# Optimization experiments

Hardware: AMD Instinct MI355X
Metric: run time of the kernel (lower is better)

The kernel has to match this reference:

```python
import jax, jax.numpy as jnp
import numpy as np

N_NODES = 100000
N_EDGES = 1600000
IN_CH = 128
HID_CH = 128
EMB_CH = 128
OUT_CH = 64


def _sage_conv(x, src, dst, W_l, b_l, W_r):
    # PyG SAGEConv (mean aggr): out = lin_l(mean_{j->i} x_j) + lin_r(x_i)
    n = x.shape[0]
    msg = x[src]                                             # [E, d] gather
    summed = jax.ops.segment_sum(msg, dst, num_segments=n)   # [N, d]
    cnt = jax.ops.segment_sum(jnp.ones((src.shape[0],), x.dtype), dst, num_segments=n)
    mean = summed / jnp.maximum(cnt, 1.0)[:, None]
    return mean @ W_l + b_l + x @ W_r


def setup_inputs() -> dict:
    key = jax.random.key(0)
    ks = jax.random.split(key, 10)
    x = jax.random.normal(ks[0], (N_NODES, IN_CH), dtype=jnp.float32)
    edge_index = jax.random.randint(ks[1], (2, N_EDGES), 0, N_NODES, dtype=jnp.int32)
    s1 = 1.0 / np.sqrt(IN_CH)
    s2 = 1.0 / np.sqrt(HID_CH)
    s3 = 1.0 / np.sqrt(EMB_CH)
    return {
        "x": x,
        "edge_index": edge_index,
        "W1l": jax.random.uniform(ks[2], (IN_CH, HID_CH), jnp.float32, -s1, s1),
        "b1": jnp.zeros((HID_CH,), jnp.float32),
        "W1r": jax.random.uniform(ks[3], (IN_CH, HID_CH), jnp.float32, -s1, s1),
        "W2l": jax.random.uniform(ks[4], (HID_CH, EMB_CH), jnp.float32, -s2, s2),
        "b2": jnp.zeros((EMB_CH,), jnp.float32),
        "W2r": jax.random.uniform(ks[5], (HID_CH, EMB_CH), jnp.float32, -s2, s2),
        "Wm": jax.random.uniform(ks[6], (EMB_CH, OUT_CH), jnp.float32, -s3, s3),
        "bm": jax.random.uniform(ks[7], (OUT_CH,), jnp.float32, -s3, s3),
    }


def reference(x, edge_index, W1l, b1, W1r, W2l, b2, W2r, Wm, bm):
    src, dst = edge_index[0], edge_index[1]
    h = jax.nn.relu(_sage_conv(x, src, dst, W1l, b1, W1r))
    emb = _sage_conv(h, src, dst, W2l, b2, W2r)
    out = emb @ Wm + bm
    # F.normalize(emb, p=2, dim=-1)
    norm = jnp.sqrt(jnp.sum(emb * emb, axis=-1, keepdims=True))
    emb_n = emb / jnp.maximum(norm, 1e-12)
    return out, emb_n
```

## Files before the change

kernel.cpp:

```cpp
#include <hip/hip_runtime.h>
#include <hip/hip_fp16.h>
#include <cstdint>
#include <cstddef>

#define N_NODES 100000
#define N_EDGES 1600000
#define BSH 6
#define BNODES 64
#define NB 1563
#define CHUNK 2048

typedef _Float16 f16x8 __attribute__((ext_vector_type(8)));
typedef float f32x4 __attribute__((ext_vector_type(4)));


__device__ __forceinline__ float h2f(ushort u) {
    __half_raw r;
    r.x = u;
    return __half2float(__half(r));
}

__device__ __forceinline__ ushort f2h(float f) {
    __half h = __float2half(f);
    return static_cast<__half_raw>(h).x;
}

__device__ __forceinline__ void acc4(float4& a, uint2 v) {
    a.x += h2f((ushort)(v.x & 0xffff));
    a.y += h2f((ushort)(v.x >> 16));
    a.z += h2f((ushort)(v.y & 0xffff));
    a.w += h2f((ushort)(v.y >> 16));
}


__global__ __launch_bounds__(256) void prep_all(
        const int* __restrict__ dst, int* __restrict__ bcnt, int E,
        const float* __restrict__ x, ushort* __restrict__ x_f16, int n4,
        const float* __restrict__ W1l, const float* __restrict__ W1r,
        const float* __restrict__ W2l, const float* __restrict__ W2r,
        const float* __restrict__ Wm,
        ushort* __restrict__ W1lT, ushort* __restrict__ W1rT,
        ushort* __restrict__ W2lT, ushort* __restrict__ W2rT,
        ushort* __restrict__ WmT) {
    int bid = blockIdx.x;
    if (bid < 256) {
        __shared__ int lh[NB];
        for (int i = threadIdx.x; i < NB; i += 256) lh[i] = 0;
        __syncthreads();
        for (int e = bid * 256 + threadIdx.x; e < E; e += 256 * 256)
            atomicAdd(&lh[dst[e] >> BSH], 1);
        __syncthreads();
        for (int i = threadIdx.x; i < NB; i += 256) {
            int v = lh[i];
            if (v) atomicAdd(&bcnt[i], v);
        }
    } else if (bid < 256 + 12500) {
        int i = (bid - 256) * 256 + threadIdx.x;
        if (i < n4) {
            float4 v = reinterpret_cast<const float4*>(x)[i];
            ushort4 o;
            o.x = f2h(v.x);
            o.y = f2h(v.y);
            o.z = f2h(v.z);
            o.w = f2h(v.w);
            reinterpret_cast<ushort4*>(x_f16)[i] = o;
        }
    } else {
        int t = (bid - (256 + 12500)) * 256 + threadIdx.x;
        if (t < 65536) {
            int wsel = t >> 14;
            int r = t & 16383;
            const float* srcs[4] = {W1l, W1r, W2l, W2r};
            ushort* dsts[4] = {W1lT, W1rT, W2lT, W2rT};
            int k = r >> 7, c = r & 127;
            dsts[wsel][c * 128 + k] = f2h(srcs[wsel][r]);
        } else if (t < 65536 + 8192) {
            int r = t - 65536;
            int k = r >> 6, c = r & 63;
            WmT[c * 128 + k] = f2h(Wm[r]);
        }
    }
}

__global__ void scan_buckets(const int* __restrict__ bcnt, int* __restrict__ boffs) {
    __shared__ int sdata[256];
    int tid = threadIdx.x;
    int v[8];
    int s = 0;
#pragma unroll
    for (int i = 0; i < 8; i++) {
        int idx = tid * 8 + i;
        v[i] = (idx < NB) ? bcnt[idx] : 0;
        s += v[i];
    }
    sdata[tid] = s;
    __syncthreads();
    int acc = s;
    for (int off = 1; off < 256; off <<= 1) {
        int t = (tid >= off) ? sdata[tid - off] : 0;
        __syncthreads();
        acc += t;
        sdata[tid] = acc;
        __syncthreads();
    }
    int excl = acc - s;
#pragma unroll
    for (int i = 0; i < 8; i++) {
        int idx = tid * 8 + i;
        if (idx < NB) boffs[idx] = excl;
        excl += v[i];
    }
}

__global__ void bucket_scatter(const int* __restrict__ src, const int* __restrict__ dst,
                               const int* __restrict__ boffs, int* __restrict__ gcur,
                               uint* __restrict__ bedges, int E) {
    __shared__ int lh[NB];
    __shared__ int lbase[NB];
    int nwg = gridDim.x;
    int chunk = (E + nwg - 1) / nwg;
    int e0 = blockIdx.x * chunk;
    int e1 = e0 + chunk;
    if (e1 > E) e1 = E;
    for (int i = threadIdx.x; i < NB; i += 256) lh[i] = 0;
    __syncthreads();
    for (int e = e0 + threadIdx.x; e < e1; e += 256)
        atomicAdd(&lh[dst[e] >> BSH], 1);
    __syncthreads();
    for (int i = threadIdx.x; i < NB; i += 256) {
        int v = lh[i];
        lbase[i] = v ? (boffs[i] + atomicAdd(&gcur[i], v)) : 0;
    }
    __syncthreads();
    for (int i = threadIdx.x; i < NB; i += 256) lh[i] = 0;
    __syncthreads();
    int e = e0 + threadIdx.x;
#pragma unroll 1
    for (; e + 3 * 256 < e1; e += 4 * 256) {
        int d0 = dst[e + 0 * 256], s0 = src[e + 0 * 256];
        int d1 = dst[e + 1 * 256], s1 = src[e + 1 * 256];
        int d2 = dst[e + 2 * 256], s2 = src[e + 2 * 256];
        int d3 = dst[e + 3 * 256], s3 = src[e + 3 * 256];
        int b0 = d0 >> BSH, b1 = d1 >> BSH, b2 = d2 >> BSH, b3 = d3 >> BSH;
        int r0 = atomicAdd(&lh[b0], 1);
        int r1 = atomicAdd(&lh[b1], 1);
        int r2 = atomicAdd(&lh[b2], 1);
        int r3 = atomicAdd(&lh[b3], 1);
        bedges[lbase[b0] + r0] = ((uint)(d0 & (BNODES - 1)) << 17) | (uint)s0;
        bedges[lbase[b1] + r1] = ((uint)(d1 & (BNODES - 1)) << 17) | (uint)s1;
        bedges[lbase[b2] + r2] = ((uint)(d2 & (BNODES - 1)) << 17) | (uint)s2;
        bedges[lbase[b3] + r3] = ((uint)(d3 & (BNODES - 1)) << 17) | (uint)s3;
    }
    for (; e < e1; e += 256) {
        int d = dst[e];
        int b = d >> BSH;
        int r = atomicAdd(&lh[b], 1);
        bedges[lbase[b] + r] = ((uint)(d & (BNODES - 1)) << 17) | (uint)src[e];
    }
}


__global__ __launch_bounds__(512) void aggregate_bucket(
        const ushort* __restrict__ F, const uint* __restrict__ bedges,
        const int* __restrict__ boffs, const int* __restrict__ bcnt,
        ushort* __restrict__ out, int n) {
    int b = blockIdx.x;
    int beg = boffs[b];
    int m = bcnt[b];
    int node0 = b << BSH;
    int nNodes = n - node0;
    if (nNodes > BNODES) nNodes = BNODES;
    __shared__ uint ls[CHUNK];
    __shared__ int lh[BNODES];
    __shared__ int lofs[BNODES];
    __shared__ int pcnt[BNODES];
    int tid = threadIdx.x;
    int wid = tid >> 6;
    int lane = tid & 63;
    int hw = lane >> 5;
    int cl = lane & 31;

    float4 acc[8];
#pragma unroll
    for (int i = 0; i < 8; i++) acc[i] = make_float4(0.f, 0.f, 0.f, 0.f);
    if (tid < BNODES) pcnt[tid] = 0;

    for (int base = 0; base < m; base += CHUNK) {
        int mm = m - base;
        if (mm > CHUNK) mm = CHUNK;
        __syncthreads();
        if (tid < BNODES) lh[tid] = 0;
        __syncthreads();
        for (int i = tid; i < mm; i += 512)
            atomicAdd(&lh[bedges[beg + base + i] >> 17], 1);
        __syncthreads();
        if (tid < BNODES) {
            int v = lh[tid];
            int s = v;
#pragma unroll
            for (int off = 1; off < 64; off <<= 1) {
                int t = __shfl_up(s, off);
                if (lane >= off) s += t;
            }
            lofs[tid] = s - v;
            pcnt[tid] += v;
            lh[tid] = 0;
        }
        __syncthreads();
        for (int i = tid; i < mm; i += 512) {
            uint p = bedges[beg + base + i];
            int k = p >> 17;
            int r = atomicAdd(&lh[k], 1);
            ls[lofs[k] + r] = p;
        }
        __syncthreads();
#pragma unroll
        for (int ki = 0; ki < 8; ki++) {
            int k = wid * 8 + ki;
            int s0 = lofs[k];
            int ck = lh[k];
            int j = hw;
            for (; j + 6 < ck; j += 8) {
                uint p0 = ls[s0 + j + 0] & 0x1FFFFu;
                uint p1 = ls[s0 + j + 2] & 0x1FFFFu;
                uint p2 = ls[s0 + j + 4] & 0x1FFFFu;
                uint p3 = ls[s0 + j + 6] & 0x1FFFFu;
                uint2 v0 = *reinterpret_cast<const uint2*>(F + (size_t)p0 * 128 + cl * 4);
                uint2 v1 = *reinterpret_cast<const uint2*>(F + (size_t)p1 * 128 + cl * 4);
                uint2 v2 = *reinterpret_cast<const uint2*>(F + (size_t)p2 * 128 + cl * 4);
                uint2 v3 = *reinterpret_cast<const uint2*>(F + (size_t)p3 * 128 + cl * 4);
                acc4(acc[ki], v0);
                acc4(acc[ki], v1);
                acc4(acc[ki], v2);
                acc4(acc[ki], v3);
            }
            for (; j < ck; j += 2) {
                uint p = ls[s0 + j] & 0x1FFFFu;
                uint2 v = *reinterpret_cast<const uint2*>(F + (size_t)p * 128 + cl * 4);
                acc4(acc[ki], v);
            }
        }
    }
    __syncthreads();
#pragma unroll
    for (int ki = 0; ki < 8; ki++) {
        acc[ki].x += __shfl_xor(acc[ki].x, 32);
        acc[ki].y += __shfl_xor(acc[ki].y, 32);
        acc[ki].z += __shfl_xor(acc[ki].z, 32);
        acc[ki].w += __shfl_xor(acc[ki].w, 32);
    }
    if (hw == 0) {
#pragma unroll
        for (int ki = 0; ki < 8; ki++) {
            int k = wid * 8 + ki;
            if (k < nNodes) {
                float inv = 1.0f / fmaxf((float)pcnt[k], 1.0f);
                uint2 o;
                o.x = (uint)f2h(acc[ki].x * inv) | ((uint)f2h(acc[ki].y * inv) << 16);
                o.y = (uint)f2h(acc[ki].z * inv) | ((uint)f2h(acc[ki].w * inv) << 16);
                *reinterpret_cast<uint2*>(out + (size_t)(node0 + k) * 128 + cl * 4) = o;
            }
        }
    }
}


template <bool RELU>
__global__ __launch_bounds__(256) void mfma_gemm(const ushort* __restrict__ A1,
                                                 const ushort* __restrict__ B1T,
                                                 const ushort* __restrict__ A2,
                                                 const ushort* __restrict__ B2T,
                                                 const float* __restrict__ bias,
                                                 ushort* __restrict__ Ch, int n) {
    int wid = threadIdx.x >> 6;
    int lane = threadIdx.x & 63;
    int row0 = blockIdx.x * 128 + wid * 32;
    int fr = lane & 15;
    int ko = (lane >> 4) * 8;

    f32x4 acc[2][8];
#pragma unroll
    for (int m = 0; m < 2; m++)
#pragma unroll
        for (int nf = 0; nf < 8; nf++) acc[m][nf] = (f32x4)0.f;

    for (int seg = 0; seg < 2; ++seg) {
        const ushort* A = seg ? A2 : A1;
        const ushort* BT = seg ? B2T : B1T;
#pragma unroll
        for (int k0 = 0; k0 < 128; k0 += 32) {
            f16x8 av[2];
#pragma unroll
            for (int m = 0; m < 2; m++) {
                int row = row0 + m * 16 + fr;
                if (row >= n) row = n - 1;
                av[m] = *reinterpret_cast<const f16x8*>(A + (size_t)row * 128 + k0 + ko);
            }
            f16x8 bv[8];
#pragma unroll
            for (int nf = 0; nf < 8; nf++)
                bv[nf] = *reinterpret_cast<const f16x8*>(BT + (size_t)(nf * 16 + fr) * 128 + k0 + ko);
#pragma unroll
            for (int m = 0; m < 2; m++)
#pragma unroll
                for (int nf = 0; nf < 8; nf++)
                    acc[m][nf] = __builtin_amdgcn_mfma_f32_16x16x32_f16(av[m], bv[nf], acc[m][nf], 0, 0, 0);
        }
    }

    int crow = (lane >> 4) * 4;
    int ccol = lane & 15;
    float bv[8];
#pragma unroll
    for (int nf = 0; nf < 8; nf++) bv[nf] = bias[nf * 16 + ccol];

#pragma unroll
    for (int m = 0; m < 2; m++) {
#pragma unroll
        for (int reg = 0; reg < 4; reg++) {
            int grow = row0 + m * 16 + crow + reg;
            if (grow < n) {
#pragma unroll
                for (int nf = 0; nf < 8; nf++) {
                    float v = acc[m][nf][reg] + bv[nf];
                    if (RELU) v = fmaxf(v, 0.f);
                    Ch[(size_t)grow * 128 + nf * 16 + ccol] = f2h(v);
                }
            }
        }
    }
}


__global__ __launch_bounds__(256) void gemm2_fused(const ushort* __restrict__ A1,
                                                   const ushort* __restrict__ B1T,
                                                   const ushort* __restrict__ A2,
                                                   const ushort* __restrict__ B2T,
                                                   const float* __restrict__ bias,
                                                   const ushort* __restrict__ WmT,
                                                   const float* __restrict__ bm,
                                                   float* __restrict__ outp,
                                                   float* __restrict__ embn, int n) {
    constexpr int LDK = 136;
    __shared__ ushort et[128 * LDK];
    int wid = threadIdx.x >> 6;
    int lane = threadIdx.x & 63;
    int row0 = blockIdx.x * 128 + wid * 32;
    int fr = lane & 15;
    int ko = (lane >> 4) * 8;

    f32x4 acc[2][8];
#pragma unroll
    for (int m = 0; m < 2; m++)
#pragma unroll
        for (int nf = 0; nf < 8; nf++) acc[m][nf] = (f32x4)0.f;

    for (int seg = 0; seg < 2; ++seg) {
        const ushort* A = seg ? A2 : A1;
        const ushort* BT = seg ? B2T : B1T;
#pragma unroll
        for (int k0 = 0; k0 < 128; k0 += 32) {
            f16x8 av[2];
#pragma unroll
            for (int m = 0; m < 2; m++) {
                int row = row0 + m * 16 + fr;
                if (row >= n) row = n - 1;
                av[m] = *reinterpret_cast<const f16x8*>(A + (size_t)row * 128 + k0 + ko);
            }
            f16x8 bv[8];
#pragma unroll
            for (int nf = 0; nf < 8; nf++)
                bv[nf] = *reinterpret_cast<const f16x8*>(BT + (size_t)(nf * 16 + fr) * 128 + k0 + ko);
#pragma unroll
            for (int m = 0; m < 2; m++)
#pragma unroll
                for (int nf = 0; nf < 8; nf++)
                    acc[m][nf] = __builtin_amdgcn_mfma_f32_16x16x32_f16(av[m], bv[nf], acc[m][nf], 0, 0, 0);
        }
    }

    int crow = (lane >> 4) * 4;
    int ccol = lane & 15;
    float bvv[8];
#pragma unroll
    for (int nf = 0; nf < 8; nf++) bvv[nf] = bias[nf * 16 + ccol];

#pragma unroll
    for (int m = 0; m < 2; m++) {
#pragma unroll
        for (int reg = 0; reg < 4; reg++) {
            float vv[8];
            float ss = 0.f;
#pragma unroll
            for (int nf = 0; nf < 8; nf++) {
                float v = acc[m][nf][reg] + bvv[nf];
                vv[nf] = v;
                ss += v * v;
            }
            ss += __shfl_xor(ss, 1);
            ss += __shfl_xor(ss, 2);
            ss += __shfl_xor(ss, 4);
            ss += __shfl_xor(ss, 8);
            float inv = 1.0f / fmaxf(sqrtf(ss), 1e-12f);
            int lrow = wid * 32 + m * 16 + crow + reg;
            int grow = blockIdx.x * 128 + lrow;
#pragma unroll
            for (int nf = 0; nf < 8; nf++)
                et[lrow * LDK + nf * 16 + ccol] = f2h(vv[nf]);
            if (grow < n) {
#pragma unroll
                for (int nf = 0; nf < 8; nf++)
                    embn[(size_t)grow * 128 + nf * 16 + ccol] = vv[nf] * inv;
            }
        }
    }
    __syncthreads();

    f32x4 acc2[2][4];
#pragma unroll
    for (int m = 0; m < 2; m++)
#pragma unroll
        for (int nf = 0; nf < 4; nf++) acc2[m][nf] = (f32x4)0.f;

#pragma unroll
    for (int k0 = 0; k0 < 128; k0 += 32) {
        f16x8 av[2];
#pragma unroll
        for (int m = 0; m < 2; m++) {
            int lrow = wid * 32 + m * 16 + fr;
            av[m] = *reinterpret_cast<const f16x8*>(&et[lrow * LDK + k0 + ko]);
        }
        f16x8 bv[4];
#pragma unroll
        for (int nf = 0; nf < 4; nf++)
            bv[nf] = *reinterpret_cast<const f16x8*>(WmT + (size_t)(nf * 16 + fr) * 128 + k0 + ko);
#pragma unroll
        for (int m = 0; m < 2; m++)
#pragma unroll
            for (int nf = 0; nf < 4; nf++)
                acc2[m][nf] = __builtin_amdgcn_mfma_f32_16x16x32_f16(av[m], bv[nf], acc2[m][nf], 0, 0, 0);
    }

#pragma unroll
    for (int m = 0; m < 2; m++) {
#pragma unroll
        for (int reg = 0; reg < 4; reg++) {
            int grow = row0 + m * 16 + crow + reg;
            if (grow < n) {
#pragma unroll
                for (int nf = 0; nf < 4; nf++)
                    outp[(size_t)grow * 64 + nf * 16 + ccol] = acc2[m][nf][reg] + bm[nf * 16 + ccol];
            }
        }
    }
}


extern "C" void kernel_launch(void* const* d_in, const int* in_sizes, int n_in,
                              void* d_out, int out_size, void* d_ws, size_t ws_size,
                              hipStream_t stream) {
    const float* x   = (const float*)d_in[0];
    const int*   ei  = (const int*)d_in[1];
    const float* W1l = (const float*)d_in[2];
    const float* b1  = (const float*)d_in[3];
    const float* W1r = (const float*)d_in[4];
    const float* W2l = (const float*)d_in[5];
    const float* b2  = (const float*)d_in[6];
    const float* W2r = (const float*)d_in[7];
    const float* Wm  = (const float*)d_in[8];
    const float* bm  = (const float*)d_in[9];

    const int N = N_NODES, E = N_EDGES;
    const int* src = ei;
    const int* dst = ei + E;

    char* ws = (char*)d_ws;
    int* bcnt  = (int*)ws;  ws += sizeof(int) * NB;
    int* boffs = (int*)ws;  ws += sizeof(int) * NB;
    int* gcur  = (int*)ws;  ws += sizeof(int) * NB;
    uintptr_t p0 = ((uintptr_t)ws + 255) & ~(uintptr_t)255;
    uint* bedges = (uint*)p0;
    uintptr_t p1 = ((uintptr_t)(bedges + N_EDGES) + 255) & ~(uintptr_t)255;
    ushort* mean_f16 = (ushort*)p1;
    ushort* x_f16    = mean_f16 + (size_t)N * 128;
    ushort* h_f16    = x_f16 + (size_t)N * 128;
    ushort* W1lT     = h_f16 + (size_t)N * 128;
    ushort* W1rT     = W1lT + 128 * 128;
    ushort* W2lT     = W1rT + 128 * 128;
    ushort* W2rT     = W2lT + 128 * 128;
    ushort* WmT      = W2rT + 128 * 128;

    float* outp = (float*)d_out;
    float* embn = outp + (size_t)N * 64;

    hipMemsetAsync(bcnt, 0, sizeof(int) * NB, stream);
    hipMemsetAsync(gcur, 0, sizeof(int) * NB, stream);

    int n4 = N * 128 / 4;
    int prep_blocks = 256 + 12500 + 288;
    prep_all<<<prep_blocks, 256, 0, stream>>>(dst, bcnt, E, x, x_f16, n4,
                                              W1l, W1r, W2l, W2r, Wm,
                                              W1lT, W1rT, W2lT, W2rT, WmT);
    scan_buckets<<<1, 256, 0, stream>>>(bcnt, boffs);
    bucket_scatter<<<256, 256, 0, stream>>>(src, dst, boffs, gcur, bedges, E);

    int gblk = (N + 127) / 128;

    aggregate_bucket<<<NB, 512, 0, stream>>>(x_f16, bedges, boffs, bcnt, mean_f16, N);
    mfma_gemm<true><<<gblk, 256, 0, stream>>>(mean_f16, W1lT, x_f16, W1rT, b1, h_f16, N);

    aggregate_bucket<<<NB, 512, 0, stream>>>(h_f16, bedges, boffs, bcnt, mean_f16, N);
    gemm2_fused<<<gblk, 256, 0, stream>>>(mean_f16, W2lT, h_f16, W2rT, b2,
                                          WmT, bm, outp, embn, N);
}
```

Measured before the change: 323.7 us.

## Fuse neighbor mean aggregation with SAGE GEMMs via LDS tiles

Each bucket block now aggregates its 64 nodes' neighbor means into an LDS tile and immediately runs the lin_l/lin_r MFMA GEMMs, bias and ReLU (layer 1), or bias, L2 normalize and the output projection (layer 2). This removes the mean_f16 round trip through global memory and two kernel launches. In exchange, the aggregation blocks grow in LDS and register use, which may lower occupancy for the gather-bound phase. Weights are also re-read per 64-node block instead of per 128-row block.

```diff
diff --git a/kernel.cpp b/kernel.cpp
--- a/kernel.cpp
+++ b/kernel.cpp
@@ -9,6 +9,7 @@
 #define BNODES 64
 #define NB 1563
 #define CHUNK 2048
+#define LDK 136
 
 typedef _Float16 f16x8 __attribute__((ext_vector_type(8)));
 typedef float f32x4 __attribute__((ext_vector_type(4)));
@@ -160,20 +161,9 @@
 }
 
 
-__global__ __launch_bounds__(512) void aggregate_bucket(
+__device__ __forceinline__ void aggregate_to_lds(
         const ushort* __restrict__ F, const uint* __restrict__ bedges,
-        const int* __restrict__ boffs, const int* __restrict__ bcnt,
-        ushort* __restrict__ out, int n) {
-    int b = blockIdx.x;
-    int beg = boffs[b];
-    int m = bcnt[b];
-    int node0 = b << BSH;
-    int nNodes = n - node0;
-    if (nNodes > BNODES) nNodes = BNODES;
-    __shared__ uint ls[CHUNK];
-    __shared__ int lh[BNODES];
-    __shared__ int lofs[BNODES];
-    __shared__ int pcnt[BNODES];
+        int beg, int m, ushort* mt, uint* ls, int* lh, int* lofs, int* pcnt) {
     int tid = threadIdx.x;
     int wid = tid >> 6;
     int lane = tid & 63;
@@ -253,203 +243,207 @@
 #pragma unroll
         for (int ki = 0; ki < 8; ki++) {
             int k = wid * 8 + ki;
-            if (k < nNodes) {
-                float inv = 1.0f / fmaxf((float)pcnt[k], 1.0f);
-                uint2 o;
-                o.x = (uint)f2h(acc[ki].x * inv) | ((uint)f2h(acc[ki].y * inv) << 16);
-                o.y = (uint)f2h(acc[ki].z * inv) | ((uint)f2h(acc[ki].w * inv) << 16);
-                *reinterpret_cast<uint2*>(out + (size_t)(node0 + k) * 128 + cl * 4) = o;
-            }
-        }
-    }
-}
-
-
-template <bool RELU>
-__global__ __launch_bounds__(256) void mfma_gemm(const ushort* __restrict__ A1,
-                                                 const ushort* __restrict__ B1T,
-                                                 const ushort* __restrict__ A2,
-                                                 const ushort* __restrict__ B2T,
-                                                 const float* __restrict__ bias,
-                                                 ushort* __restrict__ Ch, int n) {
+            float inv = 1.0f / fmaxf((float)pcnt[k], 1.0f);
+            uint2 o;
+            o.x = (uint)f2h(acc[ki].x * inv) | ((uint)f2h(acc[ki].y * inv) << 16);
+            o.y = (uint)f2h(acc[ki].z * inv) | ((uint)f2h(acc[ki].w * inv) << 16);
+            *reinterpret_cast<uint2*>(&mt[k * LDK + cl * 4]) = o;
+        }
+    }
+    __syncthreads();
+}
+
+
+__global__ __launch_bounds__(512) void agg_gemm1(
+        const ushort* __restrict__ x_f16, const uint* __restrict__ bedges,
+        const int* __restrict__ boffs, const int* __restrict__ bcnt,
+        const ushort* __restrict__ W1lT, const ushort* __restrict__ W1rT,
+        const float* __restrict__ b1, ushort* __restrict__ h_f16, int n) {
+    __shared__ uint ls[CHUNK];
+    __shared__ int lh[BNODES];
+    __shared__ int lofs[BNODES];
+    __shared__ int pcnt[BNODES];
+    __shared__ ushort mt[BNODES * LDK];
+    int b = blockIdx.x;
+    int node0 = b << BSH;
+    aggregate_to_lds(x_f16, bedges, boffs[b], bcnt[b], mt, ls, lh, lofs, pcnt);
+
     int wid = threadIdx.x >> 6;
     int lane = threadIdx.x & 63;
-    int row0 = blockIdx.x * 128 + wid * 32;
+    int rt = wid & 3;
+    int cg = wid >> 2;
     int fr = lane & 15;
     int ko = (lane >> 4) * 8;
 
-    f32x4 acc[2][8];
-#pragma unroll
-    for (int m = 0; m < 2; m++)
-#pragma unroll
-        for (int nf = 0; nf < 8; nf++) acc[m][nf] = (f32x4)0.f;
-
-    for (int seg = 0; seg < 2; ++seg) {
-        const ushort* A = seg ? A2 : A1;
-        const ushort* BT = seg ? B2T : B1T;
+    f32x4 acc[4];
+#pragma unroll
+    for (int nf = 0; nf < 4; nf++) acc[nf] = (f32x4)0.f;
+
+#pragma unroll
+    for (int k0 = 0; k0 < 128; k0 += 32) {
+        f16x8 av = *reinterpret_cast<const f16x8*>(&mt[(rt * 16 + fr) * LDK + k0 + ko]);
+#pragma unroll
+        for (int nf = 0; nf < 4; nf++) {
+            f16x8 bv = *reinterpret_cast<const f16x8*>(
+                W1lT + (size_t)(cg * 64 + nf * 16 + fr) * 128 + k0 + ko);
+            acc[nf] = __builtin_amdgcn_mfma_f32_16x16x32_f16(av, bv, acc[nf], 0, 0, 0);
+        }
+    }
+    {
+        int grow = node0 + rt * 16 + fr;
+        if (grow >= n) grow = n - 1;
 #pragma unroll
         for (int k0 = 0; k0 < 128; k0 += 32) {
-            f16x8 av[2];
-#pragma unroll
-            for (int m = 0; m < 2; m++) {
-                int row = row0 + m * 16 + fr;
-                if (row >= n) row = n - 1;
-                av[m] = *reinterpret_cast<const f16x8*>(A + (size_t)row * 128 + k0 + ko);
-            }
-            f16x8 bv[8];
-#pragma unroll
-            for (int nf = 0; nf < 8; nf++)
-                bv[nf] = *reinterpret_cast<const f16x8*>(BT + (size_t)(nf * 16 + fr) * 128 + k0 + ko);
-#pragma unroll
-            for (int m = 0; m < 2; m++)
-#pragma unroll
-                for (int nf = 0; nf < 8; nf++)
-                    acc[m][nf] = __builtin_amdgcn_mfma_f32_16x16x32_f16(av[m], bv[nf], acc[m][nf], 0, 0, 0);
+            f16x8 av = *reinterpret_cast<const f16x8*>(x_f16 + (size_t)grow * 128 + k0 + ko);
+#pragma unroll
+            for (int nf = 0; nf < 4; nf++) {
+                f16x8 bv = *reinterpret_cast<const f16x8*>(
+                    W1rT + (size_t)(cg * 64 + nf * 16 + fr) * 128 + k0 + ko);
+                acc[nf] = __builtin_amdgcn_mfma_f32_16x16x32_f16(av, bv, acc[nf], 0, 0, 0);
+            }
         }
     }
 
     int crow = (lane >> 4) * 4;
     int ccol = lane & 15;
-    float bv[8];
-#pragma unroll
-    for (int nf = 0; nf < 8; nf++) bv[nf] = bias[nf * 16 + ccol];
-
-#pragma unroll
-    for (int m = 0; m < 2; m++) {
-#pragma unroll
-        for (int reg = 0; reg < 4; reg++) {
-            int grow = row0 + m * 16 + crow + reg;
-            if (grow < n) {
-#pragma unroll
-                for (int nf = 0; nf < 8; nf++) {
-                    float v = acc[m][nf][reg] + bv[nf];
-                    if (RELU) v = fmaxf(v, 0.f);
-                    Ch[(size_t)grow * 128 + nf * 16 + ccol] = f2h(v);
-                }
-            }
-        }
-    }
-}
-
-
-__global__ __launch_bounds__(256) void gemm2_fused(const ushort* __restrict__ A1,
-                                                   const ushort* __restrict__ B1T,
-                                                   const ushort* __restrict__ A2,
-                                                   const ushort* __restrict__ B2T,
-                                                   const float* __restrict__ bias,
-                                                   const ushort* __restrict__ WmT,
-                                                   const float* __restrict__ bm,
-                                                   float* __restrict__ outp,
-                                                   float* __restrict__ embn, int n) {
-    constexpr int LDK = 136;
-    __shared__ ushort et[128 * LDK];
-    int wid = threadIdx.x >> 6;
-    int lane = threadIdx.x & 63;
-    int row0 = blockIdx.x * 128 + wid * 32;
+#pragma unroll
+    for (int reg = 0; reg < 4; reg++) {
+        int grow = node0 + rt * 16 + crow + reg;
+        if (grow < n) {
+#pragma unroll
+            for (int nf = 0; nf < 4; nf++) {
+                float v = acc[nf][reg] + b1[cg * 64 + nf * 16 + ccol];
+                v = fmaxf(v, 0.f);
+                h_f16[(size_t)grow * 128 + cg * 64 + nf * 16 + ccol] = f2h(v);
+            }
+        }
+    }
+}
+
+
+__global__ __launch_bounds__(512) void agg_gemm2(
+        const ushort* __restrict__ h_f16, const uint* __restrict__ bedges,
+        const int* __restrict__ boffs, const int* __restrict__ bcnt,
+        const ushort* __restrict__ W2lT, const ushort* __restrict__ W2rT,
+        const float* __restrict__ b2, const ushort* __restrict__ WmT,
+        const float* __restrict__ bm, float* __restrict__ outp,
+        float* __restrict__ embn, int n) {
+    __shared__ uint ls[CHUNK];
+    __shared__ int lh[BNODES];
+    __shared__ int lofs[BNODES];
+    __shared__ int pcnt[BNODES];
+    __shared__ ushort mt[BNODES * LDK];
+    __shared__ ushort et[BNODES * LDK];
+    int b = blockIdx.x;
+    int node0 = b << BSH;
+    aggregate_to_lds(h_f16, bedges, boffs[b], bcnt[b], mt, ls, lh, lofs, pcnt);
+
+    int tid = threadIdx.x;
+    int wid = tid >> 6;
+    int lane = tid & 63;
+    int rt = wid & 3;
+    int cg = wid >> 2;
     int fr = lane & 15;
     int ko = (lane >> 4) * 8;
 
-    f32x4 acc[2][8];
-#pragma unroll
-    for (int m = 0; m < 2; m++)
-#pragma unroll
-        for (int nf = 0; nf < 8; nf++) acc[m][nf] = (f32x4)0.f;
-
-    for (int seg = 0; seg < 2; ++seg) {
-        const ushort* A = seg ? A2 : A1;
-        const ushort* BT = seg ? B2T : B1T;
+    f32x4 acc[4];
+#pragma unroll
+    for (int nf = 0; nf < 4; nf++) acc[nf] = (f32x4)0.f;
+
+#pragma unroll
+    for (int k0 = 0; k0 < 128; k0 += 32) {
+        f16x8 av = *reinterpret_cast<const f16x8*>(&mt[(rt * 16 + fr) * LDK + k0 + ko]);
+#pragma unroll
+        for (int nf = 0; nf < 4; nf++) {
+            f16x8 bv = *reinterpret_cast<const f16x8*>(
+                W2lT + (size_t)(cg * 64 + nf * 16 + fr) * 128 + k0 + ko);
+            acc[nf] = __builtin_amdgcn_mfma_f32_16x16x32_f16(av, bv, acc[nf], 0, 0, 0);
+        }
+    }
+    {
+        int grow = node0 + rt * 16 + fr;
+        if (grow >= n) grow = n - 1;
 #pragma unroll
         for (int k0 = 0; k0 < 128; k0 += 32) {
-            f16x8 av[2];
-#pragma unroll
-            for (int m = 0; m < 2; m++) {
-                int row = row0 + m * 16 + fr;
-                if (row >= n) row = n - 1;
-                av[m] = *reinterpret_cast<const f16x8*>(A + (size_t)row * 128 + k0 + ko);
-            }
-            f16x8 bv[8];
-#pragma unroll
-            for (int nf = 0; nf < 8; nf++)
-                bv[nf] = *reinterpret_cast<const f16x8*>(BT + (size_t)(nf * 16 + fr) * 128 + k0 + ko);
-#pragma unroll
-            for (int m = 0; m < 2; m++)
-#pragma unroll
-                for (int nf = 0; nf < 8; nf++)
-                    acc[m][nf] = __builtin_amdgcn_mfma_f32_16x16x32_f16(av[m], bv[nf], acc[m][nf], 0, 0, 0);
+            f16x8 av = *reinterpret_cast<const f16x8*>(h_f16 + (size_t)grow * 128 + k0 + ko);
+#pragma unroll
+            for (int nf = 0; nf < 4; nf++) {
+                f16x8 bv = *reinterpret_cast<const f16x8*>(
+                    W2rT + (size_t)(cg * 64 + nf * 16 + fr) * 128 + k0 + ko);
+                acc[nf] = __builtin_amdgcn_mfma_f32_16x16x32_f16(av, bv, acc[nf], 0, 0, 0);
+            }
         }
     }
 
     int crow = (lane >> 4) * 4;
     int ccol = lane & 15;
-    float bvv[8];
-#pragma unroll
-    for (int nf = 0; nf < 8; nf++) bvv[nf] = bias[nf * 16 + ccol];
-
-#pragma unroll
-    for (int m = 0; m < 2; m++) {
+#pragma unroll
+    for (int reg = 0; reg < 4; reg++) {
+        int lrow = rt * 16 + crow + reg;
+#pragma unroll
+        for (int nf = 0; nf < 4; nf++) {
+            float v = acc[nf][reg] + b2[cg * 64 + nf * 16 + ccol];
+            et[lrow * LDK + cg * 64 + nf * 16 + ccol] = f2h(v);
+        }
+    }
+    __syncthreads();
+
+    {
+        int row = tid >> 3;
+        int p = tid & 7;
+        f16x8 e0 = *reinterpret_cast<const f16x8*>(&et[row * LDK + p * 16]);
+        f16x8 e1 = *reinterpret_cast<const f16x8*>(&et[row * LDK + p * 16 + 8]);
+        float vals[16];
+        float ss = 0.f;
+#pragma unroll
+        for (int j = 0; j < 8; j++) {
+            vals[j] = (float)e0[j];
+            vals[8 + j] = (float)e1[j];
+        }
+#pragma unroll
+        for (int j = 0; j < 16; j++) ss += vals[j] * vals[j];
+        ss += __shfl_xor(ss, 1);
+        ss += __shfl_xor(ss, 2);
+        ss += __shfl_xor(ss, 4);
+        float inv = 1.0f / fmaxf(sqrtf(ss), 1e-12f);
+        int grow = node0 + row;
+        if (grow < n) {
+            float4 o0, o1, o2, o3;
+            o0.x = vals[0] * inv;  o0.y = vals[1] * inv;  o0.z = vals[2] * inv;  o0.w = vals[3] * inv;
+            o1.x = vals[4] * inv;  o1.y = vals[5] * inv;  o1.z = vals[6] * inv;  o1.w = vals[7] * inv;
+            o2.x = vals[8] * inv;  o2.y = vals[9] * inv;  o2.z = vals[10] * inv; o2.w = vals[11] * inv;
+            o3.x = vals[12] * inv; o3.y = vals[13] * inv; o3.z = vals[14] * inv; o3.w = vals[15] * inv;
+            float* dst = embn + (size_t)grow * 128 + p * 16;
+            *reinterpret_cast<float4*>(dst + 0) = o0;
+            *reinterpret_cast<float4*>(dst + 4) = o1;
+            *reinterpret_cast<float4*>(dst + 8) = o2;
+            *reinterpret_cast<float4*>(dst + 12) = o3;
+        }
+    }
+
+    {
+        int ct2 = (wid >> 2) * 2;
+        f32x4 acc3[2];
+        acc3[0] = (f32x4)0.f;
+        acc3[1] = (f32x4)0.f;
+#pragma unroll
+        for (int k0 = 0; k0 < 128; k0 += 32) {
+            f16x8 av = *reinterpret_cast<const f16x8*>(&et[(rt * 16 + fr) * LDK + k0 + ko]);
+#pragma unroll
+            for (int nf = 0; nf < 2; nf++) {
+                f16x8 bv = *reinterpret_cast<const f16x8*>(
+                    WmT + (size_t)((ct2 + nf) * 16 + fr) * 128 + k0 + ko);
+                acc3[nf] = __builtin_amdgcn_mfma_f32_16x16x32_f16(av, bv, acc3[nf], 0, 0, 0);
+            }
+        }
 #pragma unroll
         for (int reg = 0; reg < 4; reg++) {
-            float vv[8];
-            float ss = 0.f;
-#pragma unroll
-            for (int nf = 0; nf < 8; nf++) {
-                float v = acc[m][nf][reg] + bvv[nf];
-                vv[nf] = v;
-                ss += v * v;
-            }
-            ss += __shfl_xor(ss, 1);
-            ss += __shfl_xor(ss, 2);
-            ss += __shfl_xor(ss, 4);
-            ss += __shfl_xor(ss, 8);
-            float inv = 1.0f / fmaxf(sqrtf(ss), 1e-12f);
-            int lrow = wid * 32 + m * 16 + crow + reg;
-            int grow = blockIdx.x * 128 + lrow;
-#pragma unroll
-            for (int nf = 0; nf < 8; nf++)
-                et[lrow * LDK + nf * 16 + ccol] = f2h(vv[nf]);
+            int grow = node0 + rt * 16 + crow + reg;
             if (grow < n) {
 #pragma unroll
-                for (int nf = 0; nf < 8; nf++)
-                    embn[(size_t)grow * 128 + nf * 16 + ccol] = vv[nf] * inv;
-            }
-        }
-    }
-    __syncthreads();
-
-    f32x4 acc2[2][4];
-#pragma unroll
-    for (int m = 0; m < 2; m++)
-#pragma unroll
-        for (int nf = 0; nf < 4; nf++) acc2[m][nf] = (f32x4)0.f;
-
-#pragma unroll
-    for (int k0 = 0; k0 < 128; k0 += 32) {
-        f16x8 av[2];
-#pragma unroll
-        for (int m = 0; m < 2; m++) {
-            int lrow = wid * 32 + m * 16 + fr;
-            av[m] = *reinterpret_cast<const f16x8*>(&et[lrow * LDK + k0 + ko]);
-        }
-        f16x8 bv[4];
-#pragma unroll
-        for (int nf = 0; nf < 4; nf++)
-            bv[nf] = *reinterpret_cast<const f16x8*>(WmT + (size_t)(nf * 16 + fr) * 128 + k0 + ko);
-#pragma unroll
-        for (int m = 0; m < 2; m++)
-#pragma unroll
-            for (int nf = 0; nf < 4; nf++)
-                acc2[m][nf] = __builtin_amdgcn_mfma_f32_16x16x32_f16(av[m], bv[nf], acc2[m][nf], 0, 0, 0);
-    }
-
-#pragma unroll
-    for (int m = 0; m < 2; m++) {
-#pragma unroll
-        for (int reg = 0; reg < 4; reg++) {
-            int grow = row0 + m * 16 + crow + reg;
-            if (grow < n) {
-#pragma unroll
-                for (int nf = 0; nf < 4; nf++)
-                    outp[(size_t)grow * 64 + nf * 16 + ccol] = acc2[m][nf][reg] + bm[nf * 16 + ccol];
+                for (int nf = 0; nf < 2; nf++)
+                    outp[(size_t)grow * 64 + (ct2 + nf) * 16 + ccol] =
+                        acc3[nf][reg] + bm[(ct2 + nf) * 16 + ccol];
             }
         }
     }
@@ -481,14 +475,13 @@
     uintptr_t p0 = ((uintptr_t)ws + 255) & ~(uintptr_t)255;
     uint* bedges = (uint*)p0;
     uintptr_t p1 = ((uintptr_t)(bedges + N_EDGES) + 255) & ~(uintptr_t)255;
-    ushort* mean_f16 = (ushort*)p1;
-    ushort* x_f16    = mean_f16 + (size_t)N * 128;
-    ushort* h_f16    = x_f16 + (size_t)N * 128;
-    ushort* W1lT     = h_f16 + (size_t)N * 128;
-    ushort* W1rT     = W1lT + 128 * 128;
-    ushort* W2lT     = W1rT + 128 * 128;
-    ushort* W2rT     = W2lT + 128 * 128;
-    ushort* WmT      = W2rT + 128 * 128;
+    ushort* x_f16 = (ushort*)p1;
+    ushort* h_f16 = x_f16 + (size_t)N * 128;
+    ushort* W1lT  = h_f16 + (size_t)N * 128;
+    ushort* W1rT  = W1lT + 128 * 128;
+    ushort* W2lT  = W1rT + 128 * 128;
+    ushort* W2rT  = W2lT + 128 * 128;
+    ushort* WmT   = W2rT + 128 * 128;
 
     float* outp = (float*)d_out;
     float* embn = outp + (size_t)N * 64;
@@ -504,12 +497,9 @@
     scan_buckets<<<1, 256, 0, stream>>>(bcnt, boffs);
     bucket_scatter<<<256, 256, 0, stream>>>(src, dst, boffs, gcur, bedges, E);
 
-    int gblk = (N + 127) / 128;
-
-    aggregate_bucket<<<NB, 512, 0, stream>>>(x_f16, bedges, boffs, bcnt, mean_f16, N);
-    mfma_gemm<true><<<gblk, 256, 0, stream>>>(mean_f16, W1lT, x_f16, W1rT, b1, h_f16, N);
-
-    aggregate_bucket<<<NB, 512, 0, stream>>>(h_f16, bedges, boffs, bcnt, mean_f16, N);
-    gemm2_fused<<<gblk, 256, 0, stream>>>(mean_f16, W2lT, h_f16, W2rT, b2,
-                                          WmT, bm, outp, embn, N);
-}
+    agg_gemm1<<<NB, 512, 0, stream>>>(x_f16, bedges, boffs, bcnt,
+                                      W1lT, W1rT, b1, h_f16, N);
+
+    agg_gemm2<<<NB, 512, 0, stream>>>(h_f16, bedges, boffs, bcnt,
+                                      W2lT, W2rT, b2, WmT, bm, outp, embn, N);
+}
```

Measured after the change: 358.5 us. 10.7% more time.

## Pre-pack weights in MFMA fragment order and halve GEMM row tiles

Applied to the files above, without the earlier changes.

Weights are now repacked during prep into the exact per-lane fragment order the 16x16x32 MFMA expects, so each B fragment load is a contiguous 16-byte load per lane rather than a strided row read. The GEMM kernels also change from 32 rows per wave (128 per block) to 16 rows per wave (64 per block), which doubles the grid and cuts accumulator registers. The aim is better occupancy and coalesced weight loads. The cost is that weight fragments are reloaded twice as often relative to the work done, since each wave now covers fewer rows.

```diff
diff --git a/kernel.cpp b/kernel.cpp
--- a/kernel.cpp
+++ b/kernel.cpp
@@ -9,6 +9,7 @@
 #define BNODES 64
 #define NB 1563
 #define CHUNK 2048
+#define LDK 136
 
 typedef _Float16 f16x8 __attribute__((ext_vector_type(8)));
 typedef float f32x4 __attribute__((ext_vector_type(4)));
@@ -39,9 +40,9 @@
         const float* __restrict__ W1l, const float* __restrict__ W1r,
         const float* __restrict__ W2l, const float* __restrict__ W2r,
         const float* __restrict__ Wm,
-        ushort* __restrict__ W1lT, ushort* __restrict__ W1rT,
-        ushort* __restrict__ W2lT, ushort* __restrict__ W2rT,
-        ushort* __restrict__ WmT) {
+        ushort* __restrict__ W1lP, ushort* __restrict__ W1rP,
+        ushort* __restrict__ W2lP, ushort* __restrict__ W2rP,
+        ushort* __restrict__ WmP) {
     int bid = blockIdx.x;
     if (bid < 256) {
         __shared__ int lh[NB];
@@ -69,15 +70,25 @@
         int t = (bid - (256 + 12500)) * 256 + threadIdx.x;
         if (t < 65536) {
             int wsel = t >> 14;
-            int r = t & 16383;
+            int o = t & 16383;
             const float* srcs[4] = {W1l, W1r, W2l, W2r};
-            ushort* dsts[4] = {W1lT, W1rT, W2lT, W2rT};
-            int k = r >> 7, c = r & 127;
-            dsts[wsel][c * 128 + k] = f2h(srcs[wsel][r]);
+            ushort* dsts[4] = {W1lP, W1rP, W2lP, W2rP};
+            int j = o & 7;
+            int lane = (o >> 3) & 63;
+            int kg = (o >> 9) & 3;
+            int nf = o >> 11;
+            int k = kg * 32 + (lane >> 4) * 8 + j;
+            int c = nf * 16 + (lane & 15);
+            dsts[wsel][o] = f2h(srcs[wsel][k * 128 + c]);
         } else if (t < 65536 + 8192) {
-            int r = t - 65536;
-            int k = r >> 6, c = r & 63;
-            WmT[c * 128 + k] = f2h(Wm[r]);
+            int o = t - 65536;
+            int j = o & 7;
+            int lane = (o >> 3) & 63;
+            int kg = (o >> 9) & 3;
+            int nf = o >> 11;
+            int k = kg * 32 + (lane >> 4) * 8 + j;
+            int c = nf * 16 + (lane & 15);
+            WmP[o] = f2h(Wm[k * 64 + c]);
         }
     }
 }
@@ -265,192 +276,135 @@
 }
 
 
-template <bool RELU>
-__global__ __launch_bounds__(256) void mfma_gemm(const ushort* __restrict__ A1,
-                                                 const ushort* __restrict__ B1T,
-                                                 const ushort* __restrict__ A2,
-                                                 const ushort* __restrict__ B2T,
-                                                 const float* __restrict__ bias,
-                                                 ushort* __restrict__ Ch, int n) {
+__global__ __launch_bounds__(256) void gemm1(
+        const ushort* __restrict__ A1, const ushort* __restrict__ W1lP,
+        const ushort* __restrict__ A2, const ushort* __restrict__ W1rP,
+        const float* __restrict__ b1, ushort* __restrict__ h_f16, int n) {
     int wid = threadIdx.x >> 6;
     int lane = threadIdx.x & 63;
-    int row0 = blockIdx.x * 128 + wid * 32;
+    int row0 = blockIdx.x * 64 + wid * 16;
     int fr = lane & 15;
     int ko = (lane >> 4) * 8;
-
-    f32x4 acc[2][8];
-#pragma unroll
-    for (int m = 0; m < 2; m++)
-#pragma unroll
-        for (int nf = 0; nf < 8; nf++) acc[m][nf] = (f32x4)0.f;
+    int arow = row0 + fr;
+    if (arow >= n) arow = n - 1;
+
+    f32x4 acc[8];
+#pragma unroll
+    for (int nf = 0; nf < 8; nf++) acc[nf] = (f32x4)0.f;
 
     for (int seg = 0; seg < 2; ++seg) {
         const ushort* A = seg ? A2 : A1;
-        const ushort* BT = seg ? B2T : B1T;
-#pragma unroll
-        for (int k0 = 0; k0 < 128; k0 += 32) {
-            f16x8 av[2];
-#pragma unroll
-            for (int m = 0; m < 2; m++) {
-                int row = row0 + m * 16 + fr;
-                if (row >= n) row = n - 1;
-                av[m] = *reinterpret_cast<const f16x8*>(A + (size_t)row * 128 + k0 + ko);
-            }
-            f16x8 bv[8];
-#pragma unroll
-            for (int nf = 0; nf < 8; nf++)
-                bv[nf] = *reinterpret_cast<const f16x8*>(BT + (size_t)(nf * 16 + fr) * 128 + k0 + ko);
-#pragma unroll
-            for (int m = 0; m < 2; m++)
-#pragma unroll
-                for (int nf = 0; nf < 8; nf++)
-                    acc[m][nf] = __builtin_amdgcn_mfma_f32_16x16x32_f16(av[m], bv[nf], acc[m][nf], 0, 0, 0);
+        const ushort* WP = seg ? W1rP : W1lP;
+#pragma unroll
+        for (int kg = 0; kg < 4; kg++) {
+            f16x8 av = *reinterpret_cast<const f16x8*>(A + (size_t)arow * 128 + kg * 32 + ko);
+#pragma unroll
+            for (int nf = 0; nf < 8; nf++) {
+                f16x8 bv = *reinterpret_cast<const f16x8*>(WP + (nf * 4 + kg) * 512 + lane * 8);
+                acc[nf] = __builtin_amdgcn_mfma_f32_16x16x32_f16(av, bv, acc[nf], 0, 0, 0);
+            }
         }
     }
 
     int crow = (lane >> 4) * 4;
     int ccol = lane & 15;
-    float bv[8];
-#pragma unroll
-    for (int nf = 0; nf < 8; nf++) bv[nf] = bias[nf * 16 + ccol];
-
-#pragma unroll
-    for (int m = 0; m < 2; m++) {
-#pragma unroll
-        for (int reg = 0; reg < 4; reg++) {
-            int grow = row0 + m * 16 + crow + reg;
-            if (grow < n) {
-#pragma unroll
-                for (int nf = 0; nf < 8; nf++) {
-                    float v = acc[m][nf][reg] + bv[nf];
-                    if (RELU) v = fmaxf(v, 0.f);
-                    Ch[(size_t)grow * 128 + nf * 16 + ccol] = f2h(v);
-                }
-            }
-        }
-    }
-}
-
-
-__global__ __launch_bounds__(256) void gemm2_fused(const ushort* __restrict__ A1,
-                                                   const ushort* __restrict__ B1T,
-                                                   const ushort* __restrict__ A2,
-                                                   const ushort* __restrict__ B2T,
-                                                   const float* __restrict__ bias,
-                                                   const ushort* __restrict__ WmT,
-                                                   const float* __restrict__ bm,
-                                                   float* __restrict__ outp,
-                                                   float* __restrict__ embn, int n) {
-    constexpr int LDK = 136;
-    __shared__ ushort et[128 * LDK];
+#pragma unroll
+    for (int reg = 0; reg < 4; reg++) {
+        int grow = row0 + crow + reg;
+        if (grow < n) {
+#pragma unroll
+            for (int nf = 0; nf < 8; nf++) {
+                float v = acc[nf][reg] + b1[nf * 16 + ccol];
+                v = fmaxf(v, 0.f);
+                h_f16[(size_t)grow * 128 + nf * 16 + ccol] = f2h(v);
+            }
+        }
+    }
+}
+
+
+__global__ __launch_bounds__(256) void gemm2(
+        const ushort* __restrict__ A1, const ushort* __restrict__ W2lP,
+        const ushort* __restrict__ A2, const ushort* __restrict__ W2rP,
+        const float* __restrict__ b2, const ushort* __restrict__ WmP,
+        const float* __restrict__ bm, float* __restrict__ outp,
+        float* __restrict__ embn, int n) {
+    __shared__ ushort et[64 * LDK];
     int wid = threadIdx.x >> 6;
     int lane = threadIdx.x & 63;
-    int row0 = blockIdx.x * 128 + wid * 32;
+    int row0 = blockIdx.x * 64 + wid * 16;
     int fr = lane & 15;
     int ko = (lane >> 4) * 8;
-
-    f32x4 acc[2][8];
-#pragma unroll
-    for (int m = 0; m < 2; m++)
-#pragma unroll
-        for (int nf = 0; nf < 8; nf++) acc[m][nf] = (f32x4)0.f;
+    int arow = row0 + fr;
+    if (arow >= n) arow = n - 1;
+
+    f32x4 acc[8];
+#pragma unroll
+    for (int nf = 0; nf < 8; nf++) acc[nf] = (f32x4)0.f;
 
     for (int seg = 0; seg < 2; ++seg) {
         const ushort* A = seg ? A2 : A1;
-        const ushort* BT = seg ? B2T : B1T;
-#pragma unroll
-        for (int k0 = 0; k0 < 128; k0 += 32) {
-            f16x8 av[2];
-#pragma unroll
-            for (int m = 0; m < 2; m++) {
-                int row = row0 + m * 16 + fr;
-                if (row >= n) row = n - 1;
-                av[m] = *reinterpret_cast<const f16x8*>(A + (size_t)row * 128 + k0 + ko);
-            }
-            f16x8 bv[8];
-#pragma unroll
-            for (int nf = 0; nf < 8; nf++)
-                bv[nf] = *reinterpret_cast<const f16x8*>(BT + (size_t)(nf * 16 + fr) * 128 + k0 + ko);
-#pragma unroll
-            for (int m = 0; m < 2; m++)
-#pragma unroll
-                for (int nf = 0; nf < 8; nf++)
-                    acc[m][nf] = __builtin_amdgcn_mfma_f32_16x16x32_f16(av[m], bv[nf], acc[m][nf], 0, 0, 0);
+        const ushort* WP = seg ? W2rP : W2lP;
+#pragma unroll
+        for (int kg = 0; kg < 4; kg++) {
+            f16x8 av = *reinterpret_cast<const f16x8*>(A + (size_t)arow * 128 + kg * 32 + ko);
+#pragma unroll
+            for (int nf = 0; nf < 8; nf++) {
+                f16x8 bv = *reinterpret_cast<const f16x8*>(WP + (nf * 4 + kg) * 512 + lane * 8);
+                acc[nf] = __builtin_amdgcn_mfma_f32_16x16x32_f16(av, bv, acc[nf], 0, 0, 0);
+            }
         }
     }
 
     int crow = (lane >> 4) * 4;
     int ccol = lane & 15;
-    float bvv[8];
-#pragma unroll
-    for (int nf = 0; nf < 8; nf++) bvv[nf] = bias[nf * 16 + ccol];
-
-#pragma unroll
-    for (int m = 0; m < 2; m++) {
-#pragma unroll
-        for (int reg = 0; reg < 4; reg++) {
-            float vv[8];
-            float ss = 0.f;
-#pragma unroll
-            for (int nf = 0; nf < 8; nf++) {
-                float v = acc[m][nf][reg] + bvv[nf];
-                vv[nf] = v;
-                ss += v * v;
-            }
-            ss += __shfl_xor(ss, 1);
-            ss += __shfl_xor(ss, 2);
-            ss += __shfl_xor(ss, 4);
-            ss += __shfl_xor(ss, 8);
-            float inv = 1.0f / fmaxf(sqrtf(ss), 1e-12f);
-            int lrow = wid * 32 + m * 16 + crow + reg;
-            int grow = blockIdx.x * 128 + lrow;
+#pragma unroll
+    for (int reg = 0; reg < 4; reg++) {
+        float vv[8];
+        float ss = 0.f;
+#pragma unroll
+        for (int nf = 0; nf < 8; nf++) {
+            float v = acc[nf][reg] + b2[nf * 16 + ccol];
+            vv[nf] = v;
+            ss += v * v;
+        }
+        ss += __shfl_xor(ss, 1);
+        ss += __shfl_xor(ss, 2);
+        ss += __shfl_xor(ss, 4);
+        ss += __shfl_xor(ss, 8);
+        float inv = 1.0f / fmaxf(sqrtf(ss), 1e-12f);
+        int lrow = wid * 16 + crow + reg;
+        int grow = blockIdx.x * 64 + lrow;
+#pragma unroll
+        for (int nf = 0; nf < 8; nf++)
+            et[lrow * LDK + nf * 16 + ccol] = f2h(vv[nf]);
+        if (grow < n) {
 #pragma unroll
             for (int nf = 0; nf < 8; nf++)
-                et[lrow * LDK + nf * 16 + ccol] = f2h(vv[nf]);
-            if (grow < n) {
-#pragma unroll
-                for (int nf = 0; nf < 8; nf++)
-                    embn[(size_t)grow * 128 + nf * 16 + ccol] = vv[nf] * inv;
-            }
-        }
-    }
-    __syncthreads();
-
-    f32x4 acc2[2][4];
-#pragma unroll
-    for (int m = 0; m < 2; m++)
-#pragma unroll
-        for (int nf = 0; nf < 4; nf++) acc2[m][nf] = (f32x4)0.f;
-
-#pragma unroll
-    for (int k0 = 0; k0 < 128; k0 += 32) {
-        f16x8 av[2];
-#pragma unroll
-        for (int m = 0; m < 2; m++) {
-            int lrow = wid * 32 + m * 16 + fr;
-            av[m] = *reinterpret_cast<const f16x8*>(&et[lrow * LDK + k0 + ko]);
-        }
-        f16x8 bv[4];
-#pragma unroll
-        for (int nf = 0; nf < 4; nf++)
-            bv[nf] = *reinterpret_cast<const f16x8*>(WmT + (size_t)(nf * 16 + fr) * 128 + k0 + ko);
-#pragma unroll
-        for (int m = 0; m < 2; m++)
+                embn[(size_t)grow * 128 + nf * 16 + ccol] = vv[nf] * inv;
+        }
+    }
+    __syncthreads();
+
+    f32x4 acc2[4];
+#pragma unroll
+    for (int nf = 0; nf < 4; nf++) acc2[nf] = (f32x4)0.f;
+#pragma unroll
+    for (int kg = 0; kg < 4; kg++) {
+        f16x8 av = *reinterpret_cast<const f16x8*>(&et[(wid * 16 + fr) * LDK + kg * 32 + ko]);
+#pragma unroll
+        for (int nf = 0; nf < 4; nf++) {
+            f16x8 bv = *reinterpret_cast<const f16x8*>(WmP + (nf * 4 + kg) * 512 + lane * 8);
+            acc2[nf] = __builtin_amdgcn_mfma_f32_16x16x32_f16(av, bv, acc2[nf], 0, 0, 0);
+        }
+    }
+#pragma unroll
+    for (int reg = 0; reg < 4; reg++) {
+        int grow = row0 + crow + reg;
+        if (grow < n) {
 #pragma unroll
             for (int nf = 0; nf < 4; nf++)
-                acc2[m][nf] = __builtin_amdgcn_mfma_f32_16x16x32_f16(av[m], bv[nf], acc2[m][nf], 0, 0, 0);
-    }
-
-#pragma unroll
-    for (int m = 0; m < 2; m++) {
-#pragma unroll
-        for (int reg = 0; reg < 4; reg++) {
-            int grow = row0 + m * 16 + crow + reg;
-            if (grow < n) {
-#pragma unroll
-                for (int nf = 0; nf < 4; nf++)
-                    outp[(size_t)grow * 64 + nf * 16 + ccol] = acc2[m][nf][reg] + bm[nf * 16 + ccol];
-            }
+                outp[(size_t)grow * 64 + nf * 16 + ccol] = acc2[nf][reg] + bm[nf * 16 + ccol];
         }
     }
 }
@@ -484,11 +438,11 @@
     ushort* mean_f16 = (ushort*)p1;
     ushort* x_f16    = mean_f16 + (size_t)N * 128;
     ushort* h_f16    = x_f16 + (size_t)N * 128;
-    ushort* W1lT     = h_f16 + (size_t)N * 128;
-    ushort* W1rT     = W1lT + 128 * 128;
-    ushort* W2lT     = W1rT + 128 * 128;
-    ushort* W2rT     = W2lT + 128 * 128;
-    ushort* WmT      = W2rT + 128 * 128;
+    ushort* W1lP     = h_f16 + (size_t)N * 128;
+    ushort* W1rP     = W1lP + 128 * 128;
+    ushort* W2lP     = W1rP + 128 * 128;
+    ushort* W2rP     = W2lP + 128 * 128;
+    ushort* WmP      = W2rP + 128 * 128;
 
     float* outp = (float*)d_out;
     float* embn = outp + (size_t)N * 64;
@@ -500,16 +454,16 @@
     int prep_blocks = 256 + 12500 + 288;
     prep_all<<<prep_blocks, 256, 0, stream>>>(dst, bcnt, E, x, x_f16, n4,
                                               W1l, W1r, W2l, W2r, Wm,
-                                              W1lT, W1rT, W2lT, W2rT, WmT);
+                                              W1lP, W1rP, W2lP, W2rP, WmP);
     scan_buckets<<<1, 256, 0, stream>>>(bcnt, boffs);
     bucket_scatter<<<256, 256, 0, stream>>>(src, dst, boffs, gcur, bedges, E);
 
-    int gblk = (N + 127) / 128;
+    int gblk = (N + 63) / 64;
 
     aggregate_bucket<<<NB, 512, 0, stream>>>(x_f16, bedges, boffs, bcnt, mean_f16, N);
-    mfma_gemm<true><<<gblk, 256, 0, stream>>>(mean_f16, W1lT, x_f16, W1rT, b1, h_f16, N);
+    gemm1<<<gblk, 256, 0, stream>>>(mean_f16, W1lP, x_f16, W1rP, b1, h_f16, N);
 
     aggregate_bucket<<<NB, 512, 0, stream>>>(h_f16, bedges, boffs, bcnt, mean_f16, N);
-    gemm2_fused<<<gblk, 256, 0, stream>>>(mean_f16, W2lT, h_f16, W2rT, b2,
-                                          WmT, bm, outp, embn, N);
-}
+    gemm2<<<gblk, 256, 0, stream>>>(mean_f16, W2lP, h_f16, W2rP, b2,
+                                    WmP, bm, outp, embn, N);
+}
```

Result: faster. 287.3 us (-11.3%).
